# Kernel tuning notes

Measured on AMD Instinct MI355X. Metric: run time of the kernel, lower is better.

The kernel has to match this reference:

```python
import jax, jax.numpy as jnp
import numpy as np

NA, NB, MAXNB = 100000, 200000, 6
ATOM_FDIM, BOND_FDIM, H, DEPTH = 133, 147, 300, 3


def setup_inputs() -> dict:
    key = jax.random.key(0)
    ks = jax.random.split(key, 8)
    # index 0 is the zero-padding entry (chemprop convention)
    f_atoms = jax.random.normal(ks[0], (NA, ATOM_FDIM), jnp.float32).at[0].set(0.0)
    f_bonds = jax.random.normal(ks[1], (NB, BOND_FDIM), jnp.float32).at[0].set(0.0)
    a2b = jax.random.randint(ks[2], (NA, MAXNB), 0, NB)
    b2a = jax.random.randint(ks[3], (NB,), 0, NA)
    b2revb = jax.random.randint(ks[4], (NB,), 0, NB)
    W_i = jax.random.normal(ks[5], (BOND_FDIM, H), jnp.float32) * (1.0 / np.sqrt(BOND_FDIM))
    W_h = jax.random.normal(ks[6], (H, H), jnp.float32) * (1.0 / np.sqrt(H))
    W_o = jax.random.normal(ks[7], (ATOM_FDIM + H, H), jnp.float32) * (1.0 / np.sqrt(ATOM_FDIM + H))
    b_o = jnp.zeros((H,), jnp.float32)
    return {"f_atoms": f_atoms, "f_bonds": f_bonds, "a2b": a2b, "b2a": b2a,
            "b2revb": b2revb, "W_i": W_i, "W_h": W_h, "W_o": W_o, "b_o": b_o}


def reference(f_atoms, f_bonds, a2b, b2a, b2revb, W_i, W_h, W_o, b_o):
    # bond-message D-MPNN forward (atom_messages=False, attention=False,
    # undirected=False, dropout=0 / eval mode)
    inp = f_bonds @ W_i                     # [NB, H]
    message = jax.nn.relu(inp)              # [NB, H]
    for _ in range(DEPTH - 1):
        # gather incoming bond messages per atom and sum over neighbors
        a_message = message[a2b].sum(axis=1)          # [NA, MAXNB, H] -> [NA, H]
        message = a_message[b2a] - message[b2revb]    # [NB, H]
        message = jax.nn.relu(inp + message @ W_h)
    a_message = message[a2b].sum(axis=1)              # [NA, H]
    a_input = jnp.concatenate([f_atoms, a_message], axis=1)  # [NA, ATOM_FDIM+H]
    atom_hiddens = jax.nn.relu(a_input @ W_o + b_o)   # [NA, H]
    # the per-molecule narrow loop in the original merely re-slices
    # atom_hiddens by a_scope; the concatenation of all slices == atom_hiddens
    return atom_hiddens
```

## Files before the change

kernel.cpp:

```cpp
#include <hip/hip_runtime.h>
#include <hip/hip_fp16.h>

#define NA 100000
#define NB 200000
#define MAXNB 6
#define AF 133
#define BF 147
#define H 300
#define HP 320
#define AFP 160
#define NP 320
#define KP_C 480
#define BM 128
#define BN 320
#define BK 32
#define NTH 512
#define LDK 40

typedef _Float16 f16;
typedef __attribute__((ext_vector_type(8))) _Float16 f16x8;
typedef __attribute__((ext_vector_type(4))) float f32x4;

__global__ void conv_pad_f16(const float* __restrict__ src, f16* __restrict__ dst,
                             int M, int Ks) {
  int idx = blockIdx.x * blockDim.x + threadIdx.x;
  if (idx >= M * (AFP / 8)) return;
  int r = idx / (AFP / 8);
  int c = (idx - r * (AFP / 8)) * 8;
  f16x8 o;
#pragma unroll
  for (int j = 0; j < 8; ++j) {
    int k = c + j;
    o[j] = (k < Ks) ? (f16)src[(size_t)r * Ks + k] : (f16)0.0f;
  }
  *(f16x8*)&dst[(size_t)r * AFP + c] = o;
}

__global__ void prep_w1(const float* __restrict__ Wi, const float* __restrict__ Wh,
                        f16* __restrict__ dst) {
  int idx = blockIdx.x * blockDim.x + threadIdx.x;
  if (idx >= NP * KP_C) return;
  int n = idx / KP_C, k = idx - n * KP_C;
  float v = 0.0f;
  if (n < H) {
    if (k < BF) v = Wi[(size_t)k * H + n];
    else if (k >= AFP && k < AFP + H) v = Wh[(size_t)(k - AFP) * H + n];
  }
  dst[idx] = (f16)v;
}

__global__ void prep_wo(const float* __restrict__ src, f16* __restrict__ dst) {
  int idx = blockIdx.x * blockDim.x + threadIdx.x;
  if (idx >= NP * KP_C) return;
  int n = idx / KP_C, k = idx - n * KP_C;
  int ks = -1;
  if (k < AF) ks = k;
  else if (k >= AFP && k < AFP + H) ks = AF + (k - AFP);
  float v = (n < H && ks >= 0) ? src[(size_t)ks * H + n] : 0.0f;
  dst[idx] = (f16)v;
}

__global__ void gather_sum_kernel(const f16* __restrict__ msg,
                                  const int* __restrict__ a2b,
                                  f16* __restrict__ amsg) {
  int idx = blockIdx.x * blockDim.x + threadIdx.x;
  if (idx >= NA * (HP / 8)) return;
  int a = idx / (HP / 8);
  int c = (idx - a * (HP / 8)) * 8;
  const int* nbr = &a2b[(size_t)a * MAXNB];
  float acc[8] = {0.f, 0.f, 0.f, 0.f, 0.f, 0.f, 0.f, 0.f};
#pragma unroll
  for (int t = 0; t < MAXNB; ++t) {
    int r = nbr[t];
    f16x8 v = *(const f16x8*)&msg[(size_t)r * HP + c];
#pragma unroll
    for (int j = 0; j < 8; ++j) acc[j] += (float)v[j];
  }
  f16x8 o;
#pragma unroll
  for (int j = 0; j < 8; ++j) o[j] = (f16)acc[j];
  *(f16x8*)&amsg[(size_t)a * HP + c] = o;
}

template <int MODE>
__global__ __launch_bounds__(NTH)
void gemm_kernel(const f16* __restrict__ Afp,
                 const f16* __restrict__ amsg,
                 const f16* __restrict__ msg_in,
                 const int* __restrict__ b2a,
                 const int* __restrict__ b2revb,
                 const f16* __restrict__ Wp,
                 const float* __restrict__ b_o,
                 f16* __restrict__ out_msg,
                 float* __restrict__ out_f32) {
  constexpr int KSTEPS = (MODE == 0) ? 5 : 15;
  constexpr int ASTEPS = 5;
  constexpr int M = (MODE == 2) ? NA : NB;

  __shared__ f16 As[2][BM][LDK];
  __shared__ f16 Bs[2][BN][LDK];

  const int mb = blockIdx.x;
  const int tid = threadIdx.x;
  const int lane = tid & 63, wid = tid >> 6;
  const int wr = wid >> 2, wc = wid & 3;

  f32x4 acc[4][5] = {};

  const int arow = tid >> 2;
  const int ac = (tid & 3) * 8;
  const int m_g = mb * BM + arow;
  const int mrow = (m_g < M) ? m_g : 0;

  const int bidx2 = tid + 2 * NTH;
  const int br0 = tid >> 2,            bc0 = (tid & 3) * 8;
  const int br1 = (tid + NTH) >> 2,    bc1 = ((tid + NTH) & 3) * 8;
  const int br2 = bidx2 >> 2,          bc2 = (bidx2 & 3) * 8;
  const bool b2ok = bidx2 < BN * 4;

  int ra = 0, rb = 0;
  if constexpr (MODE == 1) { ra = b2a[mrow]; rb = b2revb[mrow]; }

  f16x8 ax, ay, pw0, pw1, pw2;

  auto issue_loads = [&](int ks) {
    const int kb = ks * BK + ac;
    if constexpr (MODE == 0) {
      ax = *(const f16x8*)&Afp[(size_t)mrow * AFP + kb];
    } else if constexpr (MODE == 1) {
      if (ks < ASTEPS) {
        ax = *(const f16x8*)&Afp[(size_t)mrow * AFP + kb];
      } else {
        const int kk = kb - AFP;
        ax = *(const f16x8*)&amsg[(size_t)ra * HP + kk];
        ay = *(const f16x8*)&msg_in[(size_t)rb * HP + kk];
      }
    } else {
      ax = (ks < ASTEPS) ? *(const f16x8*)&Afp[(size_t)mrow * AFP + kb]
                         : *(const f16x8*)&amsg[(size_t)mrow * HP + (kb - AFP)];
    }
    const int kw = ks * BK;
    pw0 = *(const f16x8*)&Wp[(size_t)br0 * KP_C + kw + bc0];
    pw1 = *(const f16x8*)&Wp[(size_t)br1 * KP_C + kw + bc1];
    if (b2ok) pw2 = *(const f16x8*)&Wp[(size_t)br2 * KP_C + kw + bc2];
  };

  auto write_lds = [&](int buf, int ks) {
    f16x8 pa = ax;
    if constexpr (MODE == 1) {
      if (ks >= ASTEPS) pa = ax - ay;
    }
    *(f16x8*)&As[buf][arow][ac] = pa;
    *(f16x8*)&Bs[buf][br0][bc0] = pw0;
    *(f16x8*)&Bs[buf][br1][bc1] = pw1;
    if (b2ok) *(f16x8*)&Bs[buf][br2][bc2] = pw2;
  };

  issue_loads(0);
  write_lds(0, 0);
  issue_loads(1);
  __syncthreads();

  const int row16 = lane & 15, kh = (lane >> 4) * 8;

  for (int ks = 0; ks < KSTEPS; ++ks) {
    const int cur = ks & 1;
    f16x8 af[4], bfr[5];
#pragma unroll
    for (int m = 0; m < 4; ++m)
      af[m] = *(const f16x8*)&As[cur][wr * 64 + m * 16 + row16][kh];
#pragma unroll
    for (int n = 0; n < 5; ++n)
      bfr[n] = *(const f16x8*)&Bs[cur][wc * 80 + n * 16 + row16][kh];
#pragma unroll
    for (int m = 0; m < 4; ++m)
#pragma unroll
      for (int n = 0; n < 5; ++n)
        acc[m][n] = __builtin_amdgcn_mfma_f32_16x16x32_f16(af[m], bfr[n], acc[m][n], 0, 0, 0);

    if (ks + 1 < KSTEPS) write_lds(cur ^ 1, ks + 1);
    if (ks + 2 < KSTEPS) issue_loads(ks + 2);
    __syncthreads();
  }

  const int rquad = (lane >> 4) * 4;
#pragma unroll
  for (int m = 0; m < 4; ++m) {
#pragma unroll
    for (int n = 0; n < 5; ++n) {
      const int col = wc * 80 + n * 16 + row16;
#pragma unroll
      for (int j = 0; j < 4; ++j) {
        const int row = mb * BM + wr * 64 + m * 16 + rquad + j;
        float v = acc[m][n][j];
        if constexpr (MODE == 2) {
          if (row < M && col < H)
            out_f32[(size_t)row * H + col] = fmaxf(v + b_o[col], 0.0f);
        } else {
          if (row < M)
            out_msg[(size_t)row * HP + col] = (f16)fmaxf(v, 0.0f);
        }
      }
    }
  }
}

extern "C" void kernel_launch(void* const* d_in, const int* in_sizes, int n_in,
                              void* d_out, int out_size, void* d_ws, size_t ws_size,
                              hipStream_t stream) {
  const float* f_atoms = (const float*)d_in[0];
  const float* f_bonds = (const float*)d_in[1];
  const int*   a2b     = (const int*)d_in[2];
  const int*   b2a     = (const int*)d_in[3];
  const int*   b2revb  = (const int*)d_in[4];
  const float* W_i     = (const float*)d_in[5];
  const float* W_h     = (const float*)d_in[6];
  const float* W_o     = (const float*)d_in[7];
  const float* b_o     = (const float*)d_in[8];
  float* out = (float*)d_out;

  char* ws = (char*)d_ws;
  size_t off = 0;
  f16* msgA = (f16*)(ws + off); off += (size_t)NB * HP * 2;
  f16* msgB = (f16*)(ws + off); off += (size_t)NB * HP * 2;
  f16* amsg = (f16*)(ws + off); off += (size_t)NA * HP * 2;
  f16* fb16 = (f16*)(ws + off); off += (size_t)NB * AFP * 2;
  f16* fa16 = (f16*)(ws + off); off += (size_t)NA * AFP * 2;
  f16* W1P  = (f16*)(ws + off); off += (size_t)NP * KP_C * 2;
  f16* WoP  = (f16*)(ws + off); off += (size_t)NP * KP_C * 2;
  if (off > ws_size) return;

  prep_w1<<<(NP * KP_C + 255) / 256, 256, 0, stream>>>(W_i, W_h, W1P);
  prep_wo<<<(NP * KP_C + 255) / 256, 256, 0, stream>>>(W_o, WoP);
  conv_pad_f16<<<(NB * (AFP / 8) + 255) / 256, 256, 0, stream>>>(f_bonds, fb16, NB, BF);
  conv_pad_f16<<<(NA * (AFP / 8) + 255) / 256, 256, 0, stream>>>(f_atoms, fa16, NA, AF);

  const int gB = (NB + BM - 1) / BM;
  const int gA = (NA + BM - 1) / BM;
  dim3 gS((NA * (HP / 8) + 255) / 256);

  gemm_kernel<0><<<gB, NTH, 0, stream>>>(fb16, nullptr, nullptr,
                                         nullptr, nullptr, W1P, nullptr,
                                         msgA, nullptr);
  gather_sum_kernel<<<gS, 256, 0, stream>>>(msgA, a2b, amsg);
  gemm_kernel<1><<<gB, NTH, 0, stream>>>(fb16, amsg, msgA,
                                         b2a, b2revb, W1P, nullptr,
                                         msgB, nullptr);
  gather_sum_kernel<<<gS, 256, 0, stream>>>(msgB, a2b, amsg);
  gemm_kernel<1><<<gB, NTH, 0, stream>>>(fb16, amsg, msgB,
                                         b2a, b2revb, W1P, nullptr,
                                         msgA, nullptr);
  gather_sum_kernel<<<gS, 256, 0, stream>>>(msgA, a2b, amsg);
  gemm_kernel<2><<<gA, NTH, 0, stream>>>(fa16, amsg, nullptr,
                                         nullptr, nullptr, WoP, b_o,
                                         nullptr, out);
}
```

Measured before the change: 733.4 us.

## Cache input projection and shrink message GEMM K to W_h only

The first GEMM now writes the pre-activation input projection (f_bonds @ W_i) to an f16 buffer alongside the relu'd message. The per-depth message GEMMs then multiply only by W_h (K=320 instead of 480) and add the cached projection in the epilogue, so f_bonds @ W_i is no longer recomputed every iteration. The weight packing is split into separate W_i, W_h and W_o buffers. Workspace is reused by aliasing fb16 with amsg and fa16 with msgB, and the atom conversion is moved to after msgB's last use. In exchange, each depth step reads an extra NB x 320 f16 tensor, and the projection is rounded to f16 before the add.

```diff
diff --git a/kernel.cpp b/kernel.cpp
--- a/kernel.cpp
+++ b/kernel.cpp
@@ -10,7 +10,6 @@
 #define HP 320
 #define AFP 160
 #define NP 320
-#define KP_C 480
 #define BM 128
 #define BN 320
 #define BK 32
@@ -36,23 +35,26 @@
   *(f16x8*)&dst[(size_t)r * AFP + c] = o;
 }
 
-__global__ void prep_w1(const float* __restrict__ Wi, const float* __restrict__ Wh,
-                        f16* __restrict__ dst) {
-  int idx = blockIdx.x * blockDim.x + threadIdx.x;
-  if (idx >= NP * KP_C) return;
-  int n = idx / KP_C, k = idx - n * KP_C;
-  float v = 0.0f;
-  if (n < H) {
-    if (k < BF) v = Wi[(size_t)k * H + n];
-    else if (k >= AFP && k < AFP + H) v = Wh[(size_t)(k - AFP) * H + n];
-  }
+__global__ void prep_wi(const float* __restrict__ Wi, f16* __restrict__ dst) {
+  int idx = blockIdx.x * blockDim.x + threadIdx.x;
+  if (idx >= NP * 160) return;
+  int n = idx / 160, k = idx - n * 160;
+  float v = (n < H && k < BF) ? Wi[(size_t)k * H + n] : 0.0f;
   dst[idx] = (f16)v;
 }
 
+__global__ void prep_wh(const float* __restrict__ Wh, f16* __restrict__ dst) {
+  int idx = blockIdx.x * blockDim.x + threadIdx.x;
+  if (idx >= NP * 320) return;
+  int n = idx / 320, k = idx - n * 320;
+  float v = (n < H && k < H) ? Wh[(size_t)k * H + n] : 0.0f;
+  dst[idx] = (f16)v;
+}
+
 __global__ void prep_wo(const float* __restrict__ src, f16* __restrict__ dst) {
   int idx = blockIdx.x * blockDim.x + threadIdx.x;
-  if (idx >= NP * KP_C) return;
-  int n = idx / KP_C, k = idx - n * KP_C;
+  if (idx >= NP * 480) return;
+  int n = idx / 480, k = idx - n * 480;
   int ks = -1;
   if (k < AF) ks = k;
   else if (k >= AFP && k < AFP + H) ks = AF + (k - AFP);
@@ -90,10 +92,13 @@
                  const int* __restrict__ b2a,
                  const int* __restrict__ b2revb,
                  const f16* __restrict__ Wp,
+                 const f16* __restrict__ inp_r,
                  const float* __restrict__ b_o,
+                 f16* __restrict__ out_inp,
                  f16* __restrict__ out_msg,
                  float* __restrict__ out_f32) {
-  constexpr int KSTEPS = (MODE == 0) ? 5 : 15;
+  constexpr int KP = (MODE == 0) ? 160 : (MODE == 1) ? 320 : 480;
+  constexpr int KSTEPS = KP / BK;
   constexpr int ASTEPS = 5;
   constexpr int M = (MODE == 2) ? NA : NB;
 
@@ -128,28 +133,21 @@
     if constexpr (MODE == 0) {
       ax = *(const f16x8*)&Afp[(size_t)mrow * AFP + kb];
     } else if constexpr (MODE == 1) {
-      if (ks < ASTEPS) {
-        ax = *(const f16x8*)&Afp[(size_t)mrow * AFP + kb];
-      } else {
-        const int kk = kb - AFP;
-        ax = *(const f16x8*)&amsg[(size_t)ra * HP + kk];
-        ay = *(const f16x8*)&msg_in[(size_t)rb * HP + kk];
-      }
+      ax = *(const f16x8*)&amsg[(size_t)ra * HP + kb];
+      ay = *(const f16x8*)&msg_in[(size_t)rb * HP + kb];
     } else {
       ax = (ks < ASTEPS) ? *(const f16x8*)&Afp[(size_t)mrow * AFP + kb]
                          : *(const f16x8*)&amsg[(size_t)mrow * HP + (kb - AFP)];
     }
     const int kw = ks * BK;
-    pw0 = *(const f16x8*)&Wp[(size_t)br0 * KP_C + kw + bc0];
-    pw1 = *(const f16x8*)&Wp[(size_t)br1 * KP_C + kw + bc1];
-    if (b2ok) pw2 = *(const f16x8*)&Wp[(size_t)br2 * KP_C + kw + bc2];
+    pw0 = *(const f16x8*)&Wp[(size_t)br0 * KP + kw + bc0];
+    pw1 = *(const f16x8*)&Wp[(size_t)br1 * KP + kw + bc1];
+    if (b2ok) pw2 = *(const f16x8*)&Wp[(size_t)br2 * KP + kw + bc2];
   };
 
-  auto write_lds = [&](int buf, int ks) {
+  auto write_lds = [&](int buf) {
     f16x8 pa = ax;
-    if constexpr (MODE == 1) {
-      if (ks >= ASTEPS) pa = ax - ay;
-    }
+    if constexpr (MODE == 1) pa = ax - ay;
     *(f16x8*)&As[buf][arow][ac] = pa;
     *(f16x8*)&Bs[buf][br0][bc0] = pw0;
     *(f16x8*)&Bs[buf][br1][bc1] = pw1;
@@ -157,7 +155,7 @@
   };
 
   issue_loads(0);
-  write_lds(0, 0);
+  write_lds(0);
   issue_loads(1);
   __syncthreads();
 
@@ -178,7 +176,7 @@
       for (int n = 0; n < 5; ++n)
         acc[m][n] = __builtin_amdgcn_mfma_f32_16x16x32_f16(af[m], bfr[n], acc[m][n], 0, 0, 0);
 
-    if (ks + 1 < KSTEPS) write_lds(cur ^ 1, ks + 1);
+    if (ks + 1 < KSTEPS) write_lds(cur ^ 1);
     if (ks + 2 < KSTEPS) issue_loads(ks + 2);
     __syncthreads();
   }
@@ -196,9 +194,18 @@
         if constexpr (MODE == 2) {
           if (row < M && col < H)
             out_f32[(size_t)row * H + col] = fmaxf(v + b_o[col], 0.0f);
+        } else if constexpr (MODE == 0) {
+          if (row < M) {
+            size_t o = (size_t)row * HP + col;
+            out_inp[o] = (f16)v;
+            out_msg[o] = (f16)fmaxf(v, 0.0f);
+          }
         } else {
-          if (row < M)
-            out_msg[(size_t)row * HP + col] = (f16)fmaxf(v, 0.0f);
+          if (row < M) {
+            size_t o = (size_t)row * HP + col;
+            float x = v + (float)inp_r[o];
+            out_msg[o] = (f16)fmaxf(x, 0.0f);
+          }
         }
       }
     }
@@ -223,35 +230,38 @@
   size_t off = 0;
   f16* msgA = (f16*)(ws + off); off += (size_t)NB * HP * 2;
   f16* msgB = (f16*)(ws + off); off += (size_t)NB * HP * 2;
-  f16* amsg = (f16*)(ws + off); off += (size_t)NA * HP * 2;
-  f16* fb16 = (f16*)(ws + off); off += (size_t)NB * AFP * 2;
-  f16* fa16 = (f16*)(ws + off); off += (size_t)NA * AFP * 2;
-  f16* W1P  = (f16*)(ws + off); off += (size_t)NP * KP_C * 2;
-  f16* WoP  = (f16*)(ws + off); off += (size_t)NP * KP_C * 2;
+  f16* inp  = (f16*)(ws + off); off += (size_t)NB * HP * 2;
+  f16* fb16 = (f16*)(ws + off);
+  f16* amsg = (f16*)(ws + off); off += (size_t)NB * AFP * 2;
+  f16* fa16 = msgB;
+  f16* WiP  = (f16*)(ws + off); off += (size_t)NP * 160 * 2;
+  f16* WhP  = (f16*)(ws + off); off += (size_t)NP * 320 * 2;
+  f16* WoP  = (f16*)(ws + off); off += (size_t)NP * 480 * 2;
   if (off > ws_size) return;
 
-  prep_w1<<<(NP * KP_C + 255) / 256, 256, 0, stream>>>(W_i, W_h, W1P);
-  prep_wo<<<(NP * KP_C + 255) / 256, 256, 0, stream>>>(W_o, WoP);
+  prep_wi<<<(NP * 160 + 255) / 256, 256, 0, stream>>>(W_i, WiP);
+  prep_wh<<<(NP * 320 + 255) / 256, 256, 0, stream>>>(W_h, WhP);
+  prep_wo<<<(NP * 480 + 255) / 256, 256, 0, stream>>>(W_o, WoP);
   conv_pad_f16<<<(NB * (AFP / 8) + 255) / 256, 256, 0, stream>>>(f_bonds, fb16, NB, BF);
-  conv_pad_f16<<<(NA * (AFP / 8) + 255) / 256, 256, 0, stream>>>(f_atoms, fa16, NA, AF);
 
   const int gB = (NB + BM - 1) / BM;
   const int gA = (NA + BM - 1) / BM;
   dim3 gS((NA * (HP / 8) + 255) / 256);
 
   gemm_kernel<0><<<gB, NTH, 0, stream>>>(fb16, nullptr, nullptr,
-                                         nullptr, nullptr, W1P, nullptr,
-                                         msgA, nullptr);
+                                         nullptr, nullptr, WiP, nullptr, nullptr,
+                                         inp, msgA, nullptr);
   gather_sum_kernel<<<gS, 256, 0, stream>>>(msgA, a2b, amsg);
-  gemm_kernel<1><<<gB, NTH, 0, stream>>>(fb16, amsg, msgA,
-                                         b2a, b2revb, W1P, nullptr,
-                                         msgB, nullptr);
+  gemm_kernel<1><<<gB, NTH, 0, stream>>>(nullptr, amsg, msgA,
+                                         b2a, b2revb, WhP, inp, nullptr,
+                                         nullptr, msgB, nullptr);
   gather_sum_kernel<<<gS, 256, 0, stream>>>(msgB, a2b, amsg);
-  gemm_kernel<1><<<gB, NTH, 0, stream>>>(fb16, amsg, msgB,
-                                         b2a, b2revb, W1P, nullptr,
-                                         msgA, nullptr);
+  gemm_kernel<1><<<gB, NTH, 0, stream>>>(nullptr, amsg, msgB,
+                                         b2a, b2revb, WhP, inp, nullptr,
+                                         nullptr, msgA, nullptr);
+  conv_pad_f16<<<(NA * (AFP / 8) + 255) / 256, 256, 0, stream>>>(f_atoms, fa16, NA, AF);
   gather_sum_kernel<<<gS, 256, 0, stream>>>(msgA, a2b, amsg);
   gemm_kernel<2><<<gA, NTH, 0, stream>>>(fa16, amsg, nullptr,
-                                         nullptr, nullptr, WoP, b_o,
-                                         nullptr, out);
-}
+                                         nullptr, nullptr, WoP, nullptr, b_o,
+                                         nullptr, nullptr, out);
+}
```

After: 1.028 ms. 1.4x slower.
